# Performance work log

Hardware: AMD Instinct MI355X
Metric: run time of the kernel (lower is better)

## Reference

```python
import jax, jax.numpy as jnp
import numpy as np

B, N, NH, F = 4, 4096, 16, 8      # batch, grid cells, input points per cell, raw features
D, FF, H, PE = 256, 1024, 8, 32   # model_dim, ff_dim, n_heads, pos_emb_dim
NG, NI = 8192, 65536              # grid table size, input-point table size
SEQ = 4                           # 4 ** seq_level
HD = D // H


def layer_norm(x, g, b, eps=1e-5):
    mu = jnp.mean(x, axis=-1, keepdims=True)
    var = jnp.mean(jnp.square(x - mu), axis=-1, keepdims=True)
    return (x - mu) * jax.lax.rsqrt(var + eps) * g + b


def setup_inputs() -> dict:
    key = jax.random.key(0)
    ks = jax.random.split(key, 20)
    inp = {}
    inp["x"] = jax.random.normal(ks[0], (B, N, NH, F), jnp.float32)
    inp["grid_level_indices"] = jax.random.randint(ks[1], (B, N), 0, NG)
    inp["drop_mask"] = jax.random.bernoulli(ks[2], 0.1, (B, N))
    # buffers
    inp["input_mapping"] = jax.random.randint(ks[3], (NG, NH), 0, NI)
    inp["in_range"] = jax.random.bernoulli(ks[4], 0.95, (NG, NH))
    inp["input_coordinates"] = jax.random.uniform(ks[5], (2, NI), jnp.float32, -3.14, 3.14)
    inp["grid_coords"] = jax.random.uniform(ks[6], (2, NG), jnp.float32, -3.14, 3.14)
    # params
    inp["W_in"] = jax.random.normal(ks[7], (F, D), jnp.float32) * 0.05
    inp["b_in"] = jnp.zeros((D,), jnp.float32)
    inp["W_pe"] = jax.random.normal(ks[8], (2, PE), jnp.float32) * 0.2
    inp["W_bias"] = jax.random.normal(ks[9], (PE, H), jnp.float32) * 0.1
    inp["W_v"] = jax.random.normal(ks[10], (D, D), jnp.float32) * 0.02
    inp["W_o"] = jax.random.normal(ks[11], (D, D), jnp.float32) * 0.02
    inp["W1"] = jax.random.normal(ks[12], (D, FF), jnp.float32) * 0.02
    inp["W2"] = jax.random.normal(ks[13], (FF, D), jnp.float32) * 0.02
    inp["g1"] = jnp.ones((D,), jnp.float32)
    inp["b1"] = jnp.zeros((D,), jnp.float32)
    inp["g2"] = jnp.ones((D,), jnp.float32)
    inp["b2"] = jnp.zeros((D,), jnp.float32)
    return inp


def reference(x, grid_level_indices, drop_mask, input_mapping, in_range,
              input_coordinates, grid_coords, W_in, b_in, W_pe, W_bias,
              W_v, W_o, W1, W2, g1, b1, g2, b2):
    b, n, nh, _ = x.shape
    nq = n // SEQ
    K = SEQ * nh  # keys per group

    # input_layer.input_mlp: Linear + SiLU
    x = jax.nn.silu(x @ W_in + b_in)                       # [b,n,nh,D]

    # relative positions (polar): grid-cell coords vs gathered input-point coords
    gseq = grid_level_indices.reshape(b, nq, SEQ)
    idx = input_mapping[gseq]                              # [b,nq,4,nh]
    lon1 = grid_coords[0][gseq][..., None, None]           # [b,nq,4,1,1]
    lat1 = grid_coords[1][gseq][..., None, None]
    lon2 = input_coordinates[0][idx][:, :, None]           # [b,nq,1,4,nh]
    lat2 = input_coordinates[1][idx][:, :, None]
    dlon, dlat = lon2 - lon1, lat2 - lat1                  # [b,nq,4,4,nh]
    dist = jnp.sqrt(dlon * dlon + dlat * dlat + 1e-12)
    ang = jnp.arctan2(dlat, dlon)
    pos1 = dist.reshape(b, nq, SEQ, K)
    pos2 = ang.reshape(b, nq, SEQ, K)

    # mask: out-of-range OR dropped, broadcast across the 4 query cells
    m = (~in_range[grid_level_indices]) | drop_mask[:, :, None]  # [b,n,nh]
    m = m.reshape(b, nq, SEQ, nh)
    mask = jnp.broadcast_to(m[:, :, None], (b, nq, SEQ, SEQ, nh)).reshape(b, nq, SEQ, K)

    xs = x.reshape(b, nq, K, D)                            # kv tokens per group

    # positional bias -> attention scores (qkv_bias=False path: bias-only scores)
    pe = jax.nn.silu(jnp.stack([pos1, pos2], -1) @ W_pe)   # [b,nq,4,K,PE]
    bias = pe @ W_bias                                     # [b,nq,4,K,H]
    scores = jnp.moveaxis(bias, -1, 2)                     # [b,nq,H,4,K]
    scores = jnp.where(mask[:, :, None], -1e9, scores)
    att = jax.nn.softmax(scores, axis=-1)

    vh = (xs @ W_v).reshape(b, nq, K, H, HD)
    out = jnp.einsum('bqhtk,bqkhd->bqthd', att, vh).reshape(b, nq, SEQ, D)
    out = out @ W_o                                        # [b,nq,4,D]

    # nha_layer tail (q_res=False, dropout=0)
    h = layer_norm(out, g1, b1)
    h = layer_norm(h + jax.nn.silu(h @ W1) @ W2, g2, b2)
    return h.reshape(b, n, D)
```

## Files before the change

kernel.cpp:

```cpp
#include <hip/hip_runtime.h>

#define B_   4
#define N_   4096
#define NH_  16
#define F_   8
#define D_   256
#define FF_  1024
#define H_   8
#define PE_  32
#define NG_  8192
#define NI_  65536
#define NQ_  1024

typedef short short8 __attribute__((ext_vector_type(8)));
typedef float f32x4 __attribute__((ext_vector_type(4)));

union U8 { short8 s8; uint4 u4; };

__device__ __forceinline__ float silu_f(float v) {
  return v * __builtin_amdgcn_rcpf(1.f + __expf(-v));
}
__device__ __forceinline__ unsigned short f2bf(float f) {
  unsigned int x = __float_as_uint(f);
  unsigned int r = (x + 0x7fffu + ((x >> 16) & 1u)) >> 16;
  return (unsigned short)r;
}
__device__ __forceinline__ unsigned int cvt_pk(float a, float b) {
  unsigned int r;
  asm("v_cvt_pk_bf16_f32 %0, %1, %2" : "=v"(r) : "v"(a), "v"(b));
  return r;
}
__device__ __forceinline__ unsigned short f2bf1(float v) {
  return (unsigned short)cvt_pk(v, v);
}
__device__ __forceinline__ float bf2f(unsigned short h) {
  return __uint_as_float(((unsigned int)h) << 16);
}

__device__ __forceinline__ int detect_layout(const unsigned int* w) {
  unsigned b1 = 0, b0 = 0;
#pragma unroll
  for (int i = 0; i < 64; ++i) {
    unsigned v = w[i];
    b1 |= v & 0x0000FF00u;
    b0 |= v & 0x000000FFu;
  }
  return b1 ? 0 : (b0 ? 1 : 2);
}
__device__ __forceinline__ int read_bool(const void* p, int i, int lay) {
  if (lay == 0) return ((const unsigned char*)p)[i] != 0;
  if (lay == 1) return ((const int*)p)[i] != 0;
  return ((const float*)p)[i] != 0.0f;
}

#define WOP_OFF 0
#define W1P_OFF 65536
#define W2P_OFF (65536 + 262144)
#define WVP_OFF (65536 + 262144 + 262144)
#define WIP_OFF (65536 + 262144 + 262144 + 65536)
#define WBP_OFF (WIP_OFF + 8192)
#define WS_BASE_B ((WBP_OFF + 512) * 2)
#define DRP8_B  WS_BASE_B
#define INR8_B  (WS_BASE_B + 16384)
#define WS_MASKS_END (INR8_B + 131072)
#define ROWS_B  WS_MASKS_END
#define WS_ROWS_END (ROWS_B + 16384 * 256 * 2)
#define WS_TAIL ((65536 + 262144 + 262144) * 2)

__global__ __launch_bounds__(256) void k_pack(
    const float* __restrict__ Wo, const float* __restrict__ W1,
    const float* __restrict__ W2, const float* __restrict__ Wv,
    const float* __restrict__ Wi, const float* __restrict__ Wb,
    const void* __restrict__ drop, const void* __restrict__ inr,
    short* __restrict__ ws)
{
  int t = blockIdx.x * 256 + threadIdx.x;
  if (t < 8192) {
    int g = t & 3, n = (t >> 2) & 255, kk = t >> 10;
    int k0 = kk * 32 + g * 8;
    short8 v;
#pragma unroll
    for (int j = 0; j < 8; ++j) v[j] = (short)f2bf(Wo[(k0 + j) * 256 + n]);
    *(short8*)(ws + WOP_OFF + t * 8) = v;
  } else if (t < 40960) {
    int u = t - 8192;
    int g = u & 3, n = (u >> 2) & 1023, kk = u >> 12;
    int k0 = kk * 32 + g * 8;
    short8 v;
#pragma unroll
    for (int j = 0; j < 8; ++j) v[j] = (short)f2bf(W1[(k0 + j) * 1024 + n]);
    *(short8*)(ws + W1P_OFF + u * 8) = v;
  } else if (t < 73728) {
    int u = t - 40960;
    int g = u & 3, n = (u >> 2) & 255, kk = u >> 10;
    int k0 = kk * 32 + g * 8;
    short8 v;
#pragma unroll
    for (int j = 0; j < 8; ++j) v[j] = (short)f2bf(W2[(k0 + j) * 256 + n]);
    *(short8*)(ws + W2P_OFF + u * 8) = v;
  } else if (t < 81920) {
    int u = t - 73728;
    int g = u & 3, n = (u >> 2) & 255, kk = u >> 10;
    int k0 = kk * 32 + g * 8;
    short8 v;
#pragma unroll
    for (int j = 0; j < 8; ++j) v[j] = (short)f2bf(Wv[(k0 + j) * 256 + n]);
    *(short8*)(ws + WVP_OFF + u * 8) = v;
  } else if (t < 82944) {
    int u = t - 81920;
    int g = u & 3, n = u >> 2;
    short8 v;
#pragma unroll
    for (int j = 0; j < 8; ++j) {
      int k = g * 8 + j;
      v[j] = (k < 8) ? (short)f2bf(Wi[k * 256 + n]) : (short)0;
    }
    *(short8*)(ws + WIP_OFF + (n * 4 + g) * 8) = v;
  } else if (t < 83008) {
    int u = t - 82944;
    int g = u & 3, col = u >> 2;
    short8 v;
#pragma unroll
    for (int j = 0; j < 8; ++j) {
      int p = g * 8 + j;
      v[j] = (col < 8) ? (short)f2bf(Wb[p * 8 + col]) : (short)0;
    }
    *(short8*)(ws + WBP_OFF + (col * 4 + g) * 8) = v;
  } else if (t >= 83200) {
    int lay = detect_layout((const unsigned int*)inr);
    int t2 = t - 83200;
    char* wsb = (char*)ws;
    if (t2 < B_ * N_) {
      ((unsigned char*)(wsb + DRP8_B))[t2] =
          (unsigned char)read_bool(drop, t2, lay);
    } else if (t2 < B_ * N_ + NG_ * NH_) {
      int u = t2 - B_ * N_;
      ((unsigned char*)(wsb + INR8_B))[u] =
          (unsigned char)read_bool(inr, u, lay);
    }
  }
}

#define OFF_ATTB  32768
#define OFF_DIST  36864
#define OFF_ANG   37888
#define OFF_KLON  38912
#define OFF_KLAT  39168
#define OFF_KMSK  39424
#define OFF_GLON  39680
#define OFF_GLAT  39696

__global__ __launch_bounds__(256) void k_attn_mfma(
    const float* __restrict__ x, const int* __restrict__ gli,
    const unsigned char* __restrict__ drp8, const unsigned char* __restrict__ inr8,
    const int* __restrict__ imap, const float* __restrict__ icoord,
    const float* __restrict__ gcoord, const float* __restrict__ W_pe,
    const float* __restrict__ b_in, const short* __restrict__ WiP,
    const short* __restrict__ WbP, const short* __restrict__ WvP,
    unsigned short* __restrict__ rows, float* __restrict__ out, int userows)
{
  __shared__ __align__(16) char sm[39712];
  float* distl = (float*)(sm + OFF_DIST);
  float* angl = (float*)(sm + OFF_ANG);
  float* klon = (float*)(sm + OFF_KLON);
  float* klat = (float*)(sm + OFF_KLAT);
  int* kmask = (int*)(sm + OFF_KMSK);
  float* glon = (float*)(sm + OFF_GLON);
  float* glat = (float*)(sm + OFF_GLAT);

  const int grp = blockIdx.x;
  const int b = grp >> 10;
  const int q = grp & (NQ_ - 1);
  const int tid = threadIdx.x;
  const int w = tid >> 6;
  const int l15 = tid & 15;
  const int g = (tid & 63) >> 4;
  const int swz = (l15 & 7) << 4;

  if (tid < 64) {
    int s = tid >> 4;
    int gg = gli[b * N_ + q * 4 + s];
    if ((tid & 15) == 0) {
      glon[s] = gcoord[gg];
      glat[s] = gcoord[NG_ + gg];
    }
    int id = imap[gg * NH_ + (tid & 15)];
    klon[tid] = icoord[id];
    klat[tid] = icoord[NI_ + id];
    kmask[tid] = (inr8[gg * NH_ + (tid & 15)] == 0) |
                 (drp8[b * N_ + q * 4 + s] != 0);
  }

  {
    short8 a = {0, 0, 0, 0, 0, 0, 0, 0};
    if (g == 0) {
      const float4* xp = (const float4*)(x + (size_t)(b * N_ + q * 4) * 128);
      float4 xa = xp[(w * 16 + l15) * 2];
      float4 xc = xp[(w * 16 + l15) * 2 + 1];
      U8 u;
      u.u4.x = cvt_pk(xa.x, xa.y);
      u.u4.y = cvt_pk(xa.z, xa.w);
      u.u4.z = cvt_pk(xc.x, xc.y);
      u.u4.w = cvt_pk(xc.z, xc.w);
      a = u.s8;
    }
    const int k0 = w * 16 + g * 4;
    const int base_mlp = (l15 * 128 + k0 * 2) ^ swz;
#pragma unroll
    for (int nf = 0; nf < 16; ++nf) {
      short8 bv = *(const short8*)(WiP + ((nf * 16 + l15) * 4 + g) * 8);
      f32x4 accM = {0.f, 0.f, 0.f, 0.f};
      accM = __builtin_amdgcn_mfma_f32_16x16x32_bf16(a, bv, accM, 0, 0, 0);
      float bn = b_in[nf * 16 + l15];
      uint2 pv;
      pv.x = cvt_pk(silu_f(accM[0] + bn), silu_f(accM[1] + bn));
      pv.y = cvt_pk(silu_f(accM[2] + bn), silu_f(accM[3] + bn));
      *(uint2*)(sm + base_mlp + nf * 2048) = pv;
    }
  }
  __syncthreads();

  {
    const int t = tid >> 6, k = tid & 63;
    float dlon = klon[k] - glon[t];
    float dlat = klat[k] - glat[t];
    distl[tid] = sqrtf(dlon * dlon + dlat * dlat + 1e-12f);
    angl[tid] = atan2f(dlat, dlon);
  }
  __syncthreads();

  {
    float wpe0[8], wpe1[8];
    {
      const float4* wp = (const float4*)W_pe;
      float4 w0a = wp[g * 2], w0b = wp[g * 2 + 1];
      float4 w1a = wp[8 + g * 2], w1b = wp[8 + g * 2 + 1];
      wpe0[0] = w0a.x; wpe0[1] = w0a.y; wpe0[2] = w0a.z; wpe0[3] = w0a.w;
      wpe0[4] = w0b.x; wpe0[5] = w0b.y; wpe0[6] = w0b.z; wpe0[7] = w0b.w;
      wpe1[0] = w1a.x; wpe1[1] = w1a.y; wpe1[2] = w1a.z; wpe1[3] = w1a.w;
      wpe1[4] = w1b.x; wpe1[5] = w1b.y; wpe1[6] = w1b.z; wpe1[7] = w1b.w;
    }
    short8 wb = *(const short8*)(WbP + (l15 * 4 + g) * 8);
    f32x4 accS[4];
#pragma unroll
    for (int i = 0; i < 4; ++i) {
      int row = (w * 4 + i) * 16 + l15;
      float dd = distl[row];
      float aa = angl[row];
      float pe[8];
#pragma unroll
      for (int j = 0; j < 8; ++j)
        pe[j] = silu_f(fmaf(dd, wpe0[j], aa * wpe1[j]));
      U8 pu;
      pu.u4.x = cvt_pk(pe[0], pe[1]);
      pu.u4.y = cvt_pk(pe[2], pe[3]);
      pu.u4.z = cvt_pk(pe[4], pe[5]);
      pu.u4.w = cvt_pk(pe[6], pe[7]);
      f32x4 z = {0.f, 0.f, 0.f, 0.f};
      accS[i] = __builtin_amdgcn_mfma_f32_16x16x32_bf16(pu.s8, wb, z, 0, 0, 0);
    }
    float sv[16];
    float mx = -1e30f;
#pragma unroll
    for (int i = 0; i < 4; ++i)
#pragma unroll
      for (int r = 0; r < 4; ++r) {
        int k = i * 16 + g * 4 + r;
        float s = kmask[k] ? -1e9f : accS[i][r];
        sv[i * 4 + r] = s;
        mx = fmaxf(mx, s);
      }
    mx = fmaxf(mx, __shfl_xor(mx, 16));
    mx = fmaxf(mx, __shfl_xor(mx, 32));
    float sum = 0.f;
#pragma unroll
    for (int u = 0; u < 16; ++u) { sv[u] = __expf(sv[u] - mx); sum += sv[u]; }
    sum += __shfl_xor(sum, 16);
    sum += __shfl_xor(sum, 32);
    float inv = __builtin_amdgcn_rcpf(sum);
    if (l15 < 8) {
      int row = l15 * 4 + w;
      int base_sf = OFF_ATTB + ((row * 128 + g * 8) ^ ((row & 7) << 4));
#pragma unroll
      for (int i = 0; i < 4; ++i) {
        uint2 pv;
        pv.x = cvt_pk(sv[i * 4 + 0] * inv, sv[i * 4 + 1] * inv);
        pv.y = cvt_pk(sv[i * 4 + 2] * inv, sv[i * 4 + 3] * inv);
        *(uint2*)(sm + OFF_ATTB +
            ((row * 128 + (i * 16 + g * 4) * 2) ^ ((row & 7) << 4))) = pv;
      }
      (void)base_sf;
    }
  }
  __syncthreads();

  f32x4 accY[2][4];
  {
    f32x4 z = {0.f, 0.f, 0.f, 0.f};
#pragma unroll
    for (int mi = 0; mi < 2; ++mi)
#pragma unroll
      for (int ni = 0; ni < 4; ++ni) accY[mi][ni] = z;
  }
  {
    const int base_att = OFF_ATTB + ((l15 * 128 + g * 16) ^ swz);
    const int base_bf = ((w * 64 + l15) * 128 + g * 16) ^ swz;
#pragma unroll
    for (int kk = 0; kk < 2; ++kk) {
      const int xr = kk * 64;
      short8 a0 = *(const short8*)(sm + (base_att ^ xr));
      short8 a1 = *(const short8*)(sm + ((base_att + 2048) ^ xr));
      short8 bf[4];
#pragma unroll
      for (int ni = 0; ni < 4; ++ni)
        bf[ni] = *(const short8*)(sm + ((base_bf + ni * 2048) ^ xr));
#pragma unroll
      for (int ni = 0; ni < 4; ++ni) {
        accY[0][ni] = __builtin_amdgcn_mfma_f32_16x16x32_bf16(a0, bf[ni], accY[0][ni], 0, 0, 0);
        accY[1][ni] = __builtin_amdgcn_mfma_f32_16x16x32_bf16(a1, bf[ni], accY[1][ni], 0, 0, 0);
      }
    }
  }
  __syncthreads();

  {
    const int C6 = (g & 1) << 6;
    const int X0y = g * 2048 + (w * 64 + l15) * 2;
#pragma unroll
    for (int r = 0; r < 4; ++r) {
      const int mr = C6 ^ (r << 4);
#pragma unroll
      for (int ni = 0; ni < 4; ++ni) {
        const int t0 = (X0y + r * 512 + ni * 32) ^ mr;
        *(unsigned short*)(sm + t0) = f2bf1(accY[0][ni][r]);
        *(unsigned short*)(sm + t0 + 8192) = f2bf1(accY[1][ni][r]);
      }
    }
  }
  __syncthreads();

  {
    const int mf = w >> 1;
    f32x4 accV[4];
    {
      f32x4 z = {0.f, 0.f, 0.f, 0.f};
#pragma unroll
      for (int ni = 0; ni < 4; ++ni) accV[ni] = z;
    }
    const int base_y = ((mf * 16 + l15) * 512 + g * 16) ^ swz;
#pragma unroll
    for (int kk = 0; kk < 8; ++kk) {
      short8 a = *(const short8*)(sm + (base_y ^ (kk * 64)));
#pragma unroll
      for (int ni = 0; ni < 4; ++ni) {
        int col = w * 64 + ni * 16 + l15;
        short8 bv = *(const short8*)(WvP + ((size_t)(kk * 256 + col)) * 32 + g * 8);
        accV[ni] = __builtin_amdgcn_mfma_f32_16x16x32_bf16(a, bv, accV[ni], 0, 0, 0);
      }
    }
    float* outl = (float*)(sm + 16384);
    const int gb = (w & 1) * 2;
#pragma unroll
    for (int ni = 0; ni < 4; ++ni) {
      if (g == gb + (ni >> 1)) {
#pragma unroll
        for (int r = 0; r < 4; ++r)
          outl[r * 256 + w * 64 + ni * 16 + l15] = accV[ni][r];
      }
    }
  }
  __syncthreads();

  if (userows) {
    const float* outl = (const float*)(sm + 16384);
    unsigned* rb = (unsigned*)(rows + (size_t)grp * (4 * D_));
    int t2 = tid >> 7;
    int c2 = tid & 127;
#pragma unroll
    for (int tt = 0; tt < 2; ++tt) {
      int t = tt * 2 + t2;
      rb[t * 128 + c2] = cvt_pk(outl[t * 256 + 2 * c2],
                                outl[t * 256 + 2 * c2 + 1]);
    }
  } else {
    const float* outl = (const float*)(sm + 16384);
    float* ob = out + (size_t)grp * (4 * D_);
#pragma unroll
    for (int t = 0; t < 4; ++t) ob[t * 256 + tid] = outl[t * 256 + tid];
  }
}

__global__ __launch_bounds__(256) void k_attn_valu(
    const float* __restrict__ x, const int* __restrict__ gli,
    const void* __restrict__ drop, const int* __restrict__ imap,
    const void* __restrict__ inr, const float* __restrict__ icoord,
    const float* __restrict__ gcoord, const float* __restrict__ W_in,
    const float* __restrict__ b_in, const float* __restrict__ W_pe,
    const float* __restrict__ W_bias, const float* __restrict__ W_v,
    float* __restrict__ out)
{
  __shared__ __align__(16) float xl[512];
  __shared__ float glon[4], glat[4];
  __shared__ int gidx[4], dropf[4];
  __shared__ float klon[64], klat[64];
  __shared__ int kmask[64];
  __shared__ __align__(16) unsigned short xs[64 * D_];
  __shared__ __align__(16) float att[32 * 64];
  __shared__ __align__(16) float yl[4 * 8 * 260];

  const int grp = blockIdx.x;
  const int b = grp >> 10;
  const int q = grp & (NQ_ - 1);
  const int tid = threadIdx.x;
  const int lay = detect_layout((const unsigned int*)inr);

  if (tid < 4) {
    int g = gli[b * N_ + q * 4 + tid];
    gidx[tid] = g;
    glon[tid] = gcoord[g];
    glat[tid] = gcoord[NG_ + g];
    dropf[tid] = read_bool(drop, b * N_ + q * 4 + tid, lay);
  }
  const float* xb = x + (size_t)(b * N_ + q * 4) * (NH_ * F_);
  xl[tid] = xb[tid];
  xl[tid + 256] = xb[tid + 256];
  __syncthreads();

  if (tid < 64) {
    int s = tid >> 4;
    int g = gidx[s];
    int id = imap[g * NH_ + (tid & 15)];
    klon[tid] = icoord[id];
    klat[tid] = icoord[NI_ + id];
    kmask[tid] = (read_bool(inr, g * NH_ + (tid & 15), lay) == 0) | dropf[s];
  }
  {
    float w[8];
#pragma unroll
    for (int c = 0; c < 8; ++c) w[c] = W_in[c * D_ + tid];
    float bi = b_in[tid];
#pragma unroll 4
// ... 42 lines not shown
    float inv = 1.f / sm;
#pragma unroll
    for (int i = 0; i < 8; ++i) att[row * 64 + l8 + i * 8] = sv[i] * inv;
  }
  __syncthreads();
  {
    float acc[32];
#pragma unroll
    for (int r = 0; r < 32; ++r) acc[r] = 0.f;
    for (int k4 = 0; k4 < 64; k4 += 4) {
      float xv0 = bf2f(xs[(k4 + 0) * D_ + tid]);
      float xv1 = bf2f(xs[(k4 + 1) * D_ + tid]);
      float xv2 = bf2f(xs[(k4 + 2) * D_ + tid]);
      float xv3 = bf2f(xs[(k4 + 3) * D_ + tid]);
#pragma unroll
      for (int r = 0; r < 32; ++r) {
        float4 a = *(const float4*)&att[r * 64 + k4];
        acc[r] = fmaf(a.x, xv0, acc[r]);
        acc[r] = fmaf(a.y, xv1, acc[r]);
        acc[r] = fmaf(a.z, xv2, acc[r]);
        acc[r] = fmaf(a.w, xv3, acc[r]);
      }
    }
#pragma unroll
    for (int r = 0; r < 32; ++r)
      yl[(r & 3) * 2080 + (r >> 2) * 260 + tid] = acc[r];
  }
  __syncthreads();
  {
    const int h = tid >> 5;
    float o0 = 0.f, o1 = 0.f, o2 = 0.f, o3 = 0.f;
    for (int c = 0; c < 256; c += 4) {
      float w0 = W_v[(c + 0) * D_ + tid];
      float w1 = W_v[(c + 1) * D_ + tid];
      float w2 = W_v[(c + 2) * D_ + tid];
      float w3 = W_v[(c + 3) * D_ + tid];
      float4 y0 = *(const float4*)&yl[0 * 2080 + h * 260 + c];
      float4 y1 = *(const float4*)&yl[1 * 2080 + h * 260 + c];
      float4 y2 = *(const float4*)&yl[2 * 2080 + h * 260 + c];
      float4 y3 = *(const float4*)&yl[3 * 2080 + h * 260 + c];
      o0 = fmaf(y0.x, w0, o0); o0 = fmaf(y0.y, w1, o0); o0 = fmaf(y0.z, w2, o0); o0 = fmaf(y0.w, w3, o0);
      o1 = fmaf(y1.x, w0, o1); o1 = fmaf(y1.y, w1, o1); o1 = fmaf(y1.z, w2, o1); o1 = fmaf(y1.w, w3, o1);
      o2 = fmaf(y2.x, w0, o2); o2 = fmaf(y2.y, w1, o2); o2 = fmaf(y2.z, w2, o2); o2 = fmaf(y2.w, w3, o2);
      o3 = fmaf(y3.x, w0, o3); o3 = fmaf(y3.y, w1, o3); o3 = fmaf(y3.z, w2, o3); o3 = fmaf(y3.w, w3, o3);
    }
    float* ob = out + (size_t)grp * (4 * D_);
    ob[0 * D_ + tid] = o0;
    ob[1 * D_ + tid] = o1;
    ob[2 * D_ + tid] = o2;
    ob[3 * D_ + tid] = o3;
  }
}

template<int MI>
__device__ __forceinline__ void gemm_mfma(
    f32x4 acc[MI][4], const char* As, const short* Bp,
    int N, int kk0, int colbase, int l15, int g)
{
  const int swz = (l15 & 7) << 4;
  int baseA[MI];
#pragma unroll
  for (int mi = 0; mi < MI; ++mi)
    baseA[mi] = ((mi * 16 + l15) * 512 + g * 16) ^ swz;
#pragma unroll
  for (int kk = 0; kk < 8; ++kk) {
    short8 a[MI], bv[4];
#pragma unroll
    for (int mi = 0; mi < MI; ++mi)
      a[mi] = *(const short8*)(As + (baseA[mi] ^ (kk * 64)));
#pragma unroll
    for (int ni = 0; ni < 4; ++ni) {
      int col = colbase + ni * 16 + l15;
      size_t off = ((size_t)(kk0 + kk) * N + col) * 32 + g * 8;
      bv[ni] = *(const short8*)(Bp + off);
    }
#pragma unroll
    for (int mi = 0; mi < MI; ++mi)
#pragma unroll
      for (int ni = 0; ni < 4; ++ni)
        acc[mi][ni] = __builtin_amdgcn_mfma_f32_16x16x32_bf16(
            a[mi], bv[ni], acc[mi][ni], 0, 0, 0);
  }
}

__global__ __launch_bounds__(256) void k_tail_mfma(
    const float* __restrict__ g1v, const float* __restrict__ b1v,
    const float* __restrict__ g2v, const float* __restrict__ b2v,
    const short* __restrict__ WoP, const short* __restrict__ W1P,
    const short* __restrict__ W2P, const unsigned short* __restrict__ rowsrc,
    float* __restrict__ io, int userows)
{
  __shared__ __align__(16) unsigned short sA1[32 * 256];
  __shared__ __align__(16) unsigned short sU[32 * 256];
  __shared__ float sPs[4][32];
  __shared__ float sPss[4][32];

  const int tid = threadIdx.x;
  const int w = tid >> 6;
  const int l15 = tid & 15;
  const int g = (tid & 63) >> 4;
  float* base = io + (size_t)blockIdx.x * (32 * 256);

  const int C6 = (g & 1) << 6;
  const int X0s = g * 2048 + (w * 64 + l15) * 2;

  if (userows) {
    const unsigned short* rb = rowsrc + (size_t)blockIdx.x * (32 * 256);
#pragma unroll
    for (int i = 0; i < 8; ++i) {
      int e = (tid + 256 * i) * 4;
      int row = e >> 8, c = e & 255;
      uint2 v = *(const uint2*)(rb + e);
      int byte = (row * 512 + c * 2) ^ ((row & 7) << 4);
      *(uint2*)((char*)sU + byte) = v;
    }
  } else {
#pragma unroll
    for (int i = 0; i < 8; ++i) {
      int e = (tid + 256 * i) * 4;
      int row = e >> 8, c = e & 255;
      float4 v = *(const float4*)(base + e);
      uint2 pv;
      pv.x = cvt_pk(v.x, v.y);
      pv.y = cvt_pk(v.z, v.w);
      int byte = (row * 512 + c * 2) ^ ((row & 7) << 4);
      *(uint2*)((char*)sU + byte) = pv;
    }
  }
  __syncthreads();

  f32x4 acc[2][4];
  {
    f32x4 z = {0.f, 0.f, 0.f, 0.f};
#pragma unroll
    for (int mi = 0; mi < 2; ++mi)
#pragma unroll
      for (int ni = 0; ni < 4; ++ni) acc[mi][ni] = z;
  }
  gemm_mfma<2>(acc, (const char*)sU, WoP, 256, 0, w * 64, l15, g);

#pragma unroll
  for (int mi = 0; mi < 2; ++mi)
#pragma unroll
    for (int r = 0; r < 4; ++r) {
      float a0 = acc[mi][0][r], a1 = acc[mi][1][r], a2 = acc[mi][2][r], a3 = acc[mi][3][r];
      float s = a0 + a1 + a2 + a3;
      float ss = a0 * a0 + a1 * a1 + a2 * a2 + a3 * a3;
#pragma unroll
      for (int off = 1; off < 16; off <<= 1) {
        s += __shfl_xor(s, off);
        ss += __shfl_xor(ss, off);
      }
      if (l15 == 0) {
        int row = 16 * mi + 4 * g + r;
        sPs[w][row] = s;
        sPss[w][row] = ss;
      }
    }
  __syncthreads();

  {
    float ga[4], bb[4];
#pragma unroll
    for (int ni = 0; ni < 4; ++ni) {
      int col = 64 * w + 16 * ni + l15;
      ga[ni] = g1v[col];
      bb[ni] = b1v[col];
    }
#pragma unroll
    for (int mi = 0; mi < 2; ++mi)
#pragma unroll
      for (int r = 0; r < 4; ++r) {
        int row = 16 * mi + 4 * g + r;
        float S = sPs[0][row] + sPs[1][row] + sPs[2][row] + sPs[3][row];
        float SS = sPss[0][row] + sPss[1][row] + sPss[2][row] + sPss[3][row];
        float mu = S * (1.f / 256.f);
        float rs = rsqrtf(SS * (1.f / 256.f) - mu * mu + 1e-5f);
        const int mr = C6 ^ (r << 4);
#pragma unroll
        for (int ni = 0; ni < 4; ++ni) {
// ... 164 lines not shown
        a3[r] = fmaf(__uint_as_float(uv.z << 16), w[4], a3[r]);
        a3[r] = fmaf(__uint_as_float(uv.z & 0xffff0000u), w[5], a3[r]);
        a3[r] = fmaf(__uint_as_float(uv.w << 16), w[6], a3[r]);
        a3[r] = fmaf(__uint_as_float(uv.w & 0xffff0000u), w[7], a3[r]);
      }
    }
#pragma unroll
    for (int r = 0; r < 16; ++r) rl[r * 260 + tid] = a3[r];
  }
  __syncthreads();
  {
    const int r = tid >> 4, l = tid & 15;
    float s = 0.f, ss = 0.f;
#pragma unroll
    for (int i = 0; i < 16; ++i) { float v = rl[r * 260 + l + i * 16]; s += v; ss += v * v; }
#pragma unroll
    for (int off = 1; off < 16; off <<= 1) { s += __shfl_xor(s, off, 16); ss += __shfl_xor(ss, off, 16); }
    float mu = s * (1.f / 256.f);
    float rs = rsqrtf(ss * (1.f / 256.f) - mu * mu + 1e-5f);
#pragma unroll
    for (int i = 0; i < 16; ++i) {
      int d = l + i * 16;
      base[r * D_ + d] = (rl[r * 260 + d] - mu) * rs * g2[d] + b2[d];
    }
  }
}

extern "C" void kernel_launch(void* const* d_in, const int* in_sizes, int n_in,
                              void* d_out, int out_size, void* d_ws, size_t ws_size,
                              hipStream_t stream) {
  (void)in_sizes; (void)n_in; (void)out_size;
  const float* x = (const float*)d_in[0];
  const int* gli = (const int*)d_in[1];
  const void* drop = d_in[2];
  const int* imap = (const int*)d_in[3];
  const void* inr = d_in[4];
  const float* icoord = (const float*)d_in[5];
  const float* gcoord = (const float*)d_in[6];
  const float* W_in = (const float*)d_in[7];
  const float* b_in = (const float*)d_in[8];
  const float* W_pe = (const float*)d_in[9];
  const float* W_bias = (const float*)d_in[10];
  const float* W_v = (const float*)d_in[11];
  const float* W_o = (const float*)d_in[12];
  const float* W1 = (const float*)d_in[13];
  const float* W2 = (const float*)d_in[14];
  const float* g1 = (const float*)d_in[15];
  const float* b1 = (const float*)d_in[16];
  const float* g2 = (const float*)d_in[17];
  const float* b2 = (const float*)d_in[18];
  float* out = (float*)d_out;

  if (ws_size >= (size_t)WS_MASKS_END) {
    const int userows = (ws_size >= (size_t)WS_ROWS_END) ? 1 : 0;
    short* ws = (short*)d_ws;
    char* wsb = (char*)d_ws;
    k_pack<<<dim3(901), dim3(256), 0, stream>>>(
        W_o, W1, W2, W_v, W_in, W_bias, drop, inr, ws);
    k_attn_mfma<<<dim3(B_ * NQ_), dim3(256), 0, stream>>>(
        x, gli, (const unsigned char*)(wsb + DRP8_B),
        (const unsigned char*)(wsb + INR8_B), imap, icoord, gcoord, W_pe, b_in,
        ws + WIP_OFF, ws + WBP_OFF, ws + WVP_OFF,
        (unsigned short*)(wsb + ROWS_B), out, userows);
    k_tail_mfma<<<dim3((B_ * N_) / 32), dim3(256), 0, stream>>>(
        g1, b1, g2, b2, ws + WOP_OFF, ws + W1P_OFF, ws + W2P_OFF,
        (const unsigned short*)(wsb + ROWS_B), out, userows);
  } else if (ws_size >= (size_t)WS_TAIL) {
    short* ws = (short*)d_ws;
    k_pack<<<dim3(325), dim3(256), 0, stream>>>(
        W_o, W1, W2, W_v, W_in, W_bias, drop, inr, ws);
    k_attn_valu<<<dim3(B_ * NQ_), dim3(256), 0, stream>>>(
        x, gli, drop, imap, inr, icoord, gcoord, W_in, b_in, W_pe, W_bias, W_v, out);
    k_tail_mfma<<<dim3((B_ * N_) / 32), dim3(256), 0, stream>>>(
        g1, b1, g2, b2, ws + WOP_OFF, ws + W1P_OFF, ws + W2P_OFF,
        (const unsigned short*)0, out, 0);
  } else {
    k_attn_valu<<<dim3(B_ * NQ_), dim3(256), 0, stream>>>(
        x, gli, drop, imap, inr, icoord, gcoord, W_in, b_in, W_pe, W_bias, W_v, out);
    k_tail<<<dim3((B_ * N_) / 16), dim3(256), 0, stream>>>(
        W_o, W1, W2, g1, b1, g2, b2, out);
  }
}
```

Before: 118.1 us.

## Fuse attention and FFN tail into one kernel over four groups

Merges the attention kernel and the tail kernel (W_o, LayerNorm, FFN, LayerNorm) into a single kernel. Each block loops over four query groups, keeps their 16 output rows in shared memory as bf16, then runs the tail GEMMs on that 16-row tile. This removes the intermediate bf16 rows buffer round-trip through global memory and one kernel launch. In exchange, the tail runs with 16-row tiles (MI=1), so the packed weights are reused across fewer rows, and the grid shrinks to a quarter as many blocks with more shared memory each.

```diff
diff --git a/kernel.cpp b/kernel.cpp
--- a/kernel.cpp
+++ b/kernel.cpp
@@ -63,8 +63,6 @@
 #define DRP8_B  WS_BASE_B
 #define INR8_B  (WS_BASE_B + 16384)
 #define WS_MASKS_END (INR8_B + 131072)
-#define ROWS_B  WS_MASKS_END
-#define WS_ROWS_END (ROWS_B + 16384 * 256 * 2)
 #define WS_TAIL ((65536 + 262144 + 262144) * 2)
 
 __global__ __launch_bounds__(256) void k_pack(
@@ -141,6 +139,37 @@
   }
 }
 
+template<int MI>
+__device__ __forceinline__ void gemm_mfma(
+    f32x4 acc[MI][4], const char* As, const short* Bp,
+    int N, int kk0, int colbase, int l15, int g)
+{
+  const int swz = (l15 & 7) << 4;
+  int baseA[MI];
+#pragma unroll
+  for (int mi = 0; mi < MI; ++mi)
+    baseA[mi] = ((mi * 16 + l15) * 512 + g * 16) ^ swz;
+#pragma unroll
+  for (int kk = 0; kk < 8; ++kk) {
+    short8 a[MI], bv[4];
+#pragma unroll
+    for (int mi = 0; mi < MI; ++mi)
+      a[mi] = *(const short8*)(As + (baseA[mi] ^ (kk * 64)));
+#pragma unroll
+    for (int ni = 0; ni < 4; ++ni) {
+      int col = colbase + ni * 16 + l15;
+      size_t off = ((size_t)(kk0 + kk) * N + col) * 32 + g * 8;
+      bv[ni] = *(const short8*)(Bp + off);
+    }
+#pragma unroll
+    for (int mi = 0; mi < MI; ++mi)
+#pragma unroll
+      for (int ni = 0; ni < 4; ++ni)
+        acc[mi][ni] = __builtin_amdgcn_mfma_f32_16x16x32_bf16(
+            a[mi], bv[ni], acc[mi][ni], 0, 0, 0);
+  }
+}
+
 #define OFF_ATTB  32768
 #define OFF_DIST  36864
 #define OFF_ANG   37888
@@ -150,16 +179,23 @@
 #define OFF_GLON  39680
 #define OFF_GLAT  39696
 
-__global__ __launch_bounds__(256) void k_attn_mfma(
+__global__ __launch_bounds__(256) void k_fused(
     const float* __restrict__ x, const int* __restrict__ gli,
     const unsigned char* __restrict__ drp8, const unsigned char* __restrict__ inr8,
     const int* __restrict__ imap, const float* __restrict__ icoord,
     const float* __restrict__ gcoord, const float* __restrict__ W_pe,
     const float* __restrict__ b_in, const short* __restrict__ WiP,
     const short* __restrict__ WbP, const short* __restrict__ WvP,
-    unsigned short* __restrict__ rows, float* __restrict__ out, int userows)
+    const short* __restrict__ WoP, const short* __restrict__ W1P,
+    const short* __restrict__ W2P, const float* __restrict__ g1v,
+    const float* __restrict__ b1v, const float* __restrict__ g2v,
+    const float* __restrict__ b2v, float* __restrict__ out)
 {
   __shared__ __align__(16) char sm[39712];
+  __shared__ __align__(16) unsigned short sX[16 * 256];
+  __shared__ float sPs[4][16];
+  __shared__ float sPss[4][16];
+
   float* distl = (float*)(sm + OFF_DIST);
   float* angl = (float*)(sm + OFF_ANG);
   float* klon = (float*)(sm + OFF_KLON);
@@ -168,225 +204,331 @@
   float* glon = (float*)(sm + OFF_GLON);
   float* glat = (float*)(sm + OFF_GLAT);
 
-  const int grp = blockIdx.x;
-  const int b = grp >> 10;
-  const int q = grp & (NQ_ - 1);
   const int tid = threadIdx.x;
   const int w = tid >> 6;
   const int l15 = tid & 15;
   const int g = (tid & 63) >> 4;
   const int swz = (l15 & 7) << 4;
 
-  if (tid < 64) {
-    int s = tid >> 4;
-    int gg = gli[b * N_ + q * 4 + s];
-    if ((tid & 15) == 0) {
-      glon[s] = gcoord[gg];
-      glat[s] = gcoord[NG_ + gg];
-    }
-    int id = imap[gg * NH_ + (tid & 15)];
-    klon[tid] = icoord[id];
-    klat[tid] = icoord[NI_ + id];
-    kmask[tid] = (inr8[gg * NH_ + (tid & 15)] == 0) |
-                 (drp8[b * N_ + q * 4 + s] != 0);
-  }
-
-  {
-    short8 a = {0, 0, 0, 0, 0, 0, 0, 0};
-    if (g == 0) {
-      const float4* xp = (const float4*)(x + (size_t)(b * N_ + q * 4) * 128);
-      float4 xa = xp[(w * 16 + l15) * 2];
-      float4 xc = xp[(w * 16 + l15) * 2 + 1];
-      U8 u;
-      u.u4.x = cvt_pk(xa.x, xa.y);
-      u.u4.y = cvt_pk(xa.z, xa.w);
-      u.u4.z = cvt_pk(xc.x, xc.y);
-      u.u4.w = cvt_pk(xc.z, xc.w);
-      a = u.s8;
-    }
-    const int k0 = w * 16 + g * 4;
-    const int base_mlp = (l15 * 128 + k0 * 2) ^ swz;
-#pragma unroll
-    for (int nf = 0; nf < 16; ++nf) {
-      short8 bv = *(const short8*)(WiP + ((nf * 16 + l15) * 4 + g) * 8);
-      f32x4 accM = {0.f, 0.f, 0.f, 0.f};
-      accM = __builtin_amdgcn_mfma_f32_16x16x32_bf16(a, bv, accM, 0, 0, 0);
-      float bn = b_in[nf * 16 + l15];
-      uint2 pv;
-      pv.x = cvt_pk(silu_f(accM[0] + bn), silu_f(accM[1] + bn));
-      pv.y = cvt_pk(silu_f(accM[2] + bn), silu_f(accM[3] + bn));
-      *(uint2*)(sm + base_mlp + nf * 2048) = pv;
-    }
-  }
-  __syncthreads();
-
-  {
-    const int t = tid >> 6, k = tid & 63;
-    float dlon = klon[k] - glon[t];
-    float dlat = klat[k] - glat[t];
-    distl[tid] = sqrtf(dlon * dlon + dlat * dlat + 1e-12f);
-    angl[tid] = atan2f(dlat, dlon);
-  }
-  __syncthreads();
-
-  {
-    float wpe0[8], wpe1[8];
+  float wpe0[8], wpe1[8];
+  {
+    const float4* wp = (const float4*)W_pe;
+    float4 w0a = wp[g * 2], w0b = wp[g * 2 + 1];
+    float4 w1a = wp[8 + g * 2], w1b = wp[8 + g * 2 + 1];
+    wpe0[0] = w0a.x; wpe0[1] = w0a.y; wpe0[2] = w0a.z; wpe0[3] = w0a.w;
+    wpe0[4] = w0b.x; wpe0[5] = w0b.y; wpe0[6] = w0b.z; wpe0[7] = w0b.w;
+    wpe1[0] = w1a.x; wpe1[1] = w1a.y; wpe1[2] = w1a.z; wpe1[3] = w1a.w;
+    wpe1[4] = w1b.x; wpe1[5] = w1b.y; wpe1[6] = w1b.z; wpe1[7] = w1b.w;
+  }
+  const short8 wbias = *(const short8*)(WbP + (l15 * 4 + g) * 8);
+
+  for (int gi = 0; gi < 4; ++gi) {
+    const int grp = blockIdx.x * 4 + gi;
+    const int b = grp >> 10;
+    const int q = grp & (NQ_ - 1);
+
+    if (tid < 64) {
+      int s = tid >> 4;
+      int gg = gli[b * N_ + q * 4 + s];
+      if ((tid & 15) == 0) {
+        glon[s] = gcoord[gg];
+        glat[s] = gcoord[NG_ + gg];
+      }
+      int id = imap[gg * NH_ + (tid & 15)];
+      klon[tid] = icoord[id];
+      klat[tid] = icoord[NI_ + id];
+      kmask[tid] = (inr8[gg * NH_ + (tid & 15)] == 0) |
+                   (drp8[b * N_ + q * 4 + s] != 0);
+    }
+
     {
-      const float4* wp = (const float4*)W_pe;
-      float4 w0a = wp[g * 2], w0b = wp[g * 2 + 1];
-      float4 w1a = wp[8 + g * 2], w1b = wp[8 + g * 2 + 1];
-      wpe0[0] = w0a.x; wpe0[1] = w0a.y; wpe0[2] = w0a.z; wpe0[3] = w0a.w;
-      wpe0[4] = w0b.x; wpe0[5] = w0b.y; wpe0[6] = w0b.z; wpe0[7] = w0b.w;
-      wpe1[0] = w1a.x; wpe1[1] = w1a.y; wpe1[2] = w1a.z; wpe1[3] = w1a.w;
-      wpe1[4] = w1b.x; wpe1[5] = w1b.y; wpe1[6] = w1b.z; wpe1[7] = w1b.w;
-    }
-    short8 wb = *(const short8*)(WbP + (l15 * 4 + g) * 8);
-    f32x4 accS[4];
-#pragma unroll
-    for (int i = 0; i < 4; ++i) {
-      int row = (w * 4 + i) * 16 + l15;
-      float dd = distl[row];
-      float aa = angl[row];
-      float pe[8];
-#pragma unroll
-      for (int j = 0; j < 8; ++j)
-        pe[j] = silu_f(fmaf(dd, wpe0[j], aa * wpe1[j]));
-      U8 pu;
-      pu.u4.x = cvt_pk(pe[0], pe[1]);
-      pu.u4.y = cvt_pk(pe[2], pe[3]);
-      pu.u4.z = cvt_pk(pe[4], pe[5]);
-      pu.u4.w = cvt_pk(pe[6], pe[7]);
+      short8 a = {0, 0, 0, 0, 0, 0, 0, 0};
+      if (g == 0) {
+        const float4* xp = (const float4*)(x + (size_t)(b * N_ + q * 4) * 128);
+        float4 xa = xp[(w * 16 + l15) * 2];
+        float4 xc = xp[(w * 16 + l15) * 2 + 1];
+        U8 u;
+        u.u4.x = cvt_pk(xa.x, xa.y);
+        u.u4.y = cvt_pk(xa.z, xa.w);
+        u.u4.z = cvt_pk(xc.x, xc.y);
+        u.u4.w = cvt_pk(xc.z, xc.w);
+        a = u.s8;
+      }
+      const int k0 = w * 16 + g * 4;
+      const int base_mlp = (l15 * 128 + k0 * 2) ^ swz;
+#pragma unroll
+      for (int nf = 0; nf < 16; ++nf) {
+        short8 bv = *(const short8*)(WiP + ((nf * 16 + l15) * 4 + g) * 8);
+        f32x4 accM = {0.f, 0.f, 0.f, 0.f};
+        accM = __builtin_amdgcn_mfma_f32_16x16x32_bf16(a, bv, accM, 0, 0, 0);
+        float bn = b_in[nf * 16 + l15];
+        uint2 pv;
+        pv.x = cvt_pk(silu_f(accM[0] + bn), silu_f(accM[1] + bn));
+        pv.y = cvt_pk(silu_f(accM[2] + bn), silu_f(accM[3] + bn));
+        *(uint2*)(sm + base_mlp + nf * 2048) = pv;
+      }
+    }
+    __syncthreads();
+
+    {
+      const int t = tid >> 6, k = tid & 63;
+      float dlon = klon[k] - glon[t];
+      float dlat = klat[k] - glat[t];
+      distl[tid] = sqrtf(dlon * dlon + dlat * dlat + 1e-12f);
+      angl[tid] = atan2f(dlat, dlon);
+    }
+    __syncthreads();
+
+    {
+      f32x4 accS[4];
+#pragma unroll
+      for (int i = 0; i < 4; ++i) {
+        int row = (w * 4 + i) * 16 + l15;
+        float dd = distl[row];
+        float aa = angl[row];
+        float pe[8];
+#pragma unroll
+        for (int j = 0; j < 8; ++j)
+          pe[j] = silu_f(fmaf(dd, wpe0[j], aa * wpe1[j]));
+        U8 pu;
+        pu.u4.x = cvt_pk(pe[0], pe[1]);
+        pu.u4.y = cvt_pk(pe[2], pe[3]);
+        pu.u4.z = cvt_pk(pe[4], pe[5]);
+        pu.u4.w = cvt_pk(pe[6], pe[7]);
+        f32x4 z = {0.f, 0.f, 0.f, 0.f};
+        accS[i] = __builtin_amdgcn_mfma_f32_16x16x32_bf16(pu.s8, wbias, z, 0, 0, 0);
+      }
+      float sv[16];
+      float mx = -1e30f;
+#pragma unroll
+      for (int i = 0; i < 4; ++i)
+#pragma unroll
+        for (int r = 0; r < 4; ++r) {
+          int k = i * 16 + g * 4 + r;
+          float s = kmask[k] ? -1e9f : accS[i][r];
+          sv[i * 4 + r] = s;
+          mx = fmaxf(mx, s);
+        }
+      mx = fmaxf(mx, __shfl_xor(mx, 16));
+      mx = fmaxf(mx, __shfl_xor(mx, 32));
+      float sum = 0.f;
+#pragma unroll
+      for (int u = 0; u < 16; ++u) { sv[u] = __expf(sv[u] - mx); sum += sv[u]; }
+      sum += __shfl_xor(sum, 16);
+      sum += __shfl_xor(sum, 32);
+      float inv = __builtin_amdgcn_rcpf(sum);
+      if (l15 < 8) {
+        int row = l15 * 4 + w;
+        int rs = (row & 7) << 4;
+#pragma unroll
+        for (int i = 0; i < 4; ++i) {
+          uint2 pv;
+          pv.x = cvt_pk(sv[i * 4 + 0] * inv, sv[i * 4 + 1] * inv);
+          pv.y = cvt_pk(sv[i * 4 + 2] * inv, sv[i * 4 + 3] * inv);
+          *(uint2*)(sm + OFF_ATTB +
+              ((row * 128 + (i * 16 + g * 4) * 2) ^ rs)) = pv;
+        }
+      }
+    }
+    __syncthreads();
+
+    f32x4 accY[2][4];
+    {
       f32x4 z = {0.f, 0.f, 0.f, 0.f};
-      accS[i] = __builtin_amdgcn_mfma_f32_16x16x32_bf16(pu.s8, wb, z, 0, 0, 0);
-    }
-    float sv[16];
-    float mx = -1e30f;
-#pragma unroll
-    for (int i = 0; i < 4; ++i)
+#pragma unroll
+      for (int mi = 0; mi < 2; ++mi)
+#pragma unroll
+        for (int ni = 0; ni < 4; ++ni) accY[mi][ni] = z;
+    }
+    {
+      const int base_att = OFF_ATTB + ((l15 * 128 + g * 16) ^ swz);
+      const int base_bf = ((w * 64 + l15) * 128 + g * 16) ^ swz;
+#pragma unroll
+      for (int kk = 0; kk < 2; ++kk) {
+        const int xr = kk * 64;
+        short8 a0 = *(const short8*)(sm + (base_att ^ xr));
+        short8 a1 = *(const short8*)(sm + ((base_att + 2048) ^ xr));
+        short8 bf[4];
+#pragma unroll
+        for (int ni = 0; ni < 4; ++ni)
+          bf[ni] = *(const short8*)(sm + ((base_bf + ni * 2048) ^ xr));
+#pragma unroll
+        for (int ni = 0; ni < 4; ++ni) {
+          accY[0][ni] = __builtin_amdgcn_mfma_f32_16x16x32_bf16(a0, bf[ni], accY[0][ni], 0, 0, 0);
+          accY[1][ni] = __builtin_amdgcn_mfma_f32_16x16x32_bf16(a1, bf[ni], accY[1][ni], 0, 0, 0);
+        }
+      }
+    }
+    __syncthreads();
+
+    {
+      const int C6 = (g & 1) << 6;
+      const int X0y = g * 2048 + (w * 64 + l15) * 2;
 #pragma unroll
       for (int r = 0; r < 4; ++r) {
-        int k = i * 16 + g * 4 + r;
-        float s = kmask[k] ? -1e9f : accS[i][r];
-        sv[i * 4 + r] = s;
-        mx = fmaxf(mx, s);
-      }
-    mx = fmaxf(mx, __shfl_xor(mx, 16));
-    mx = fmaxf(mx, __shfl_xor(mx, 32));
-    float sum = 0.f;
-#pragma unroll
-    for (int u = 0; u < 16; ++u) { sv[u] = __expf(sv[u] - mx); sum += sv[u]; }
-    sum += __shfl_xor(sum, 16);
-    sum += __shfl_xor(sum, 32);
-    float inv = __builtin_amdgcn_rcpf(sum);
-    if (l15 < 8) {
-      int row = l15 * 4 + w;
-      int base_sf = OFF_ATTB + ((row * 128 + g * 8) ^ ((row & 7) << 4));
-#pragma unroll
-      for (int i = 0; i < 4; ++i) {
-        uint2 pv;
-        pv.x = cvt_pk(sv[i * 4 + 0] * inv, sv[i * 4 + 1] * inv);
-        pv.y = cvt_pk(sv[i * 4 + 2] * inv, sv[i * 4 + 3] * inv);
-        *(uint2*)(sm + OFF_ATTB +
-            ((row * 128 + (i * 16 + g * 4) * 2) ^ ((row & 7) << 4))) = pv;
-      }
-      (void)base_sf;
-    }
-  }
-  __syncthreads();
-
-  f32x4 accY[2][4];
+        const int mr = C6 ^ (r << 4);
+#pragma unroll
+        for (int ni = 0; ni < 4; ++ni) {
+          const int t0 = (X0y + r * 512 + ni * 32) ^ mr;
+          *(unsigned short*)(sm + t0) = f2bf1(accY[0][ni][r]);
+          *(unsigned short*)(sm + t0 + 8192) = f2bf1(accY[1][ni][r]);
+        }
+      }
+    }
+    __syncthreads();
+
+    {
+      const int mf = w >> 1;
+      f32x4 accV[4];
+      {
+        f32x4 z = {0.f, 0.f, 0.f, 0.f};
+#pragma unroll
+        for (int ni = 0; ni < 4; ++ni) accV[ni] = z;
+      }
+      const int base_y = ((mf * 16 + l15) * 512 + g * 16) ^ swz;
+#pragma unroll
+      for (int kk = 0; kk < 8; ++kk) {
+        short8 a = *(const short8*)(sm + (base_y ^ (kk * 64)));
+#pragma unroll
+        for (int ni = 0; ni < 4; ++ni) {
+          int col = w * 64 + ni * 16 + l15;
+          short8 bv = *(const short8*)(WvP + ((size_t)(kk * 256 + col)) * 32 + g * 8);
+          accV[ni] = __builtin_amdgcn_mfma_f32_16x16x32_bf16(a, bv, accV[ni], 0, 0, 0);
+        }
+      }
+      const int gb = (w & 1) * 2;
+#pragma unroll
+      for (int ni = 0; ni < 4; ++ni) {
+        if (g == gb + (ni >> 1)) {
+          int col = w * 64 + ni * 16 + l15;
+#pragma unroll
+          for (int r = 0; r < 4; ++r) {
+            int row = gi * 4 + r;
+            int byte = (row * 512 + col * 2) ^ ((row & 7) << 4);
+            *(unsigned short*)((char*)sX + byte) = f2bf1(accV[ni][r]);
+          }
+        }
+      }
+    }
+    __syncthreads();
+  }
+
+  const int C6 = (g & 1) << 6;
+  const int X0s = g * 2048 + (w * 64 + l15) * 2;
+
+  f32x4 acc[1][4];
   {
     f32x4 z = {0.f, 0.f, 0.f, 0.f};
 #pragma unroll
-    for (int mi = 0; mi < 2; ++mi)
-#pragma unroll
-      for (int ni = 0; ni < 4; ++ni) accY[mi][ni] = z;
-  }
-  {
-    const int base_att = OFF_ATTB + ((l15 * 128 + g * 16) ^ swz);
-    const int base_bf = ((w * 64 + l15) * 128 + g * 16) ^ swz;
-#pragma unroll
-    for (int kk = 0; kk < 2; ++kk) {
-      const int xr = kk * 64;
-      short8 a0 = *(const short8*)(sm + (base_att ^ xr));
-      short8 a1 = *(const short8*)(sm + ((base_att + 2048) ^ xr));
-      short8 bf[4];
-#pragma unroll
-      for (int ni = 0; ni < 4; ++ni)
-        bf[ni] = *(const short8*)(sm + ((base_bf + ni * 2048) ^ xr));
+    for (int ni = 0; ni < 4; ++ni) acc[0][ni] = z;
+  }
+  gemm_mfma<1>(acc, (const char*)sX, WoP, 256, 0, w * 64, l15, g);
+
+#pragma unroll
+  for (int r = 0; r < 4; ++r) {
+    float a0 = acc[0][0][r], a1 = acc[0][1][r], a2 = acc[0][2][r], a3 = acc[0][3][r];
+    float s = a0 + a1 + a2 + a3;
+    float ss = a0 * a0 + a1 * a1 + a2 * a2 + a3 * a3;
+#pragma unroll
+    for (int off = 1; off < 16; off <<= 1) {
+      s += __shfl_xor(s, off);
+      ss += __shfl_xor(ss, off);
+    }
+    if (l15 == 0) {
+      int row = 4 * g + r;
+      sPs[w][row] = s;
+      sPss[w][row] = ss;
+    }
+  }
+  __syncthreads();
+
+  {
+    float ga[4], bb[4];
+#pragma unroll
+    for (int ni = 0; ni < 4; ++ni) {
+      int col = 64 * w + 16 * ni + l15;
+      ga[ni] = g1v[col];
+      bb[ni] = b1v[col];
+    }
+#pragma unroll
+    for (int r = 0; r < 4; ++r) {
+      int row = 4 * g + r;
+      float S = sPs[0][row] + sPs[1][row] + sPs[2][row] + sPs[3][row];
+      float SS = sPss[0][row] + sPss[1][row] + sPss[2][row] + sPss[3][row];
+      float mu = S * (1.f / 256.f);
+      float rs = rsqrtf(SS * (1.f / 256.f) - mu * mu + 1e-5f);
+      const int mr = C6 ^ (r << 4);
 #pragma unroll
       for (int ni = 0; ni < 4; ++ni) {
-        accY[0][ni] = __builtin_amdgcn_mfma_f32_16x16x32_bf16(a0, bf[ni], accY[0][ni], 0, 0, 0);
-        accY[1][ni] = __builtin_amdgcn_mfma_f32_16x16x32_bf16(a1, bf[ni], accY[1][ni], 0, 0, 0);
-      }
-    }
-  }
-  __syncthreads();
-
-  {
-    const int C6 = (g & 1) << 6;
-    const int X0y = g * 2048 + (w * 64 + l15) * 2;
+        float val = (acc[0][ni][r] - mu) * rs * ga[ni] + bb[ni];
+        acc[0][ni][r] = val;
+        *(unsigned short*)(sm + ((X0s + r * 512 + ni * 32) ^ mr)) = f2bf1(val);
+      }
+    }
+  }
+  __syncthreads();
+
+  for (int p = 0; p < 4; ++p) {
+    f32x4 acc2[1][4];
+    {
+      f32x4 z = {0.f, 0.f, 0.f, 0.f};
+#pragma unroll
+      for (int ni = 0; ni < 4; ++ni) acc2[0][ni] = z;
+    }
+    gemm_mfma<1>(acc2, (const char*)sm, W1P, 1024, 0, p * 256 + w * 64, l15, g);
 #pragma unroll
     for (int r = 0; r < 4; ++r) {
       const int mr = C6 ^ (r << 4);
 #pragma unroll
+      for (int ni = 0; ni < 4; ++ni)
+        *(unsigned short*)(sm + 8192 + ((X0s + r * 512 + ni * 32) ^ mr)) =
+            f2bf1(silu_f(acc2[0][ni][r]));
+    }
+    __syncthreads();
+    gemm_mfma<1>(acc, (const char*)(sm + 8192), W2P, 256, p * 8, w * 64, l15, g);
+    __syncthreads();
+  }
+
+#pragma unroll
+  for (int r = 0; r < 4; ++r) {
+    float a0 = acc[0][0][r], a1 = acc[0][1][r], a2 = acc[0][2][r], a3 = acc[0][3][r];
+    float s = a0 + a1 + a2 + a3;
+    float ss = a0 * a0 + a1 * a1 + a2 * a2 + a3 * a3;
+#pragma unroll
+    for (int off = 1; off < 16; off <<= 1) {
+      s += __shfl_xor(s, off);
+      ss += __shfl_xor(ss, off);
+    }
+    if (l15 == 0) {
+      int row = 4 * g + r;
+      sPs[w][row] = s;
+      sPss[w][row] = ss;
+    }
+  }
+  __syncthreads();
+
+  {
+    float* base = out + (size_t)blockIdx.x * (16 * 256);
+    float ga[4], bb[4];
+#pragma unroll
+    for (int ni = 0; ni < 4; ++ni) {
+      int col = 64 * w + 16 * ni + l15;
+      ga[ni] = g2v[col];
+      bb[ni] = b2v[col];
+    }
+#pragma unroll
+    for (int r = 0; r < 4; ++r) {
+      int row = 4 * g + r;
+      float S = sPs[0][row] + sPs[1][row] + sPs[2][row] + sPs[3][row];
+      float SS = sPss[0][row] + sPss[1][row] + sPss[2][row] + sPss[3][row];
+      float mu = S * (1.f / 256.f);
+      float rs = rsqrtf(SS * (1.f / 256.f) - mu * mu + 1e-5f);
+#pragma unroll
       for (int ni = 0; ni < 4; ++ni) {
-        const int t0 = (X0y + r * 512 + ni * 32) ^ mr;
-        *(unsigned short*)(sm + t0) = f2bf1(accY[0][ni][r]);
-        *(unsigned short*)(sm + t0 + 8192) = f2bf1(accY[1][ni][r]);
-      }
-    }
-  }
-  __syncthreads();
-
-  {
-    const int mf = w >> 1;
-    f32x4 accV[4];
-    {
-      f32x4 z = {0.f, 0.f, 0.f, 0.f};
-#pragma unroll
-      for (int ni = 0; ni < 4; ++ni) accV[ni] = z;
-    }
-    const int base_y = ((mf * 16 + l15) * 512 + g * 16) ^ swz;
-#pragma unroll
-    for (int kk = 0; kk < 8; ++kk) {
-      short8 a = *(const short8*)(sm + (base_y ^ (kk * 64)));
-#pragma unroll
-      for (int ni = 0; ni < 4; ++ni) {
-        int col = w * 64 + ni * 16 + l15;
-        short8 bv = *(const short8*)(WvP + ((size_t)(kk * 256 + col)) * 32 + g * 8);
-        accV[ni] = __builtin_amdgcn_mfma_f32_16x16x32_bf16(a, bv, accV[ni], 0, 0, 0);
-      }
-    }
-    float* outl = (float*)(sm + 16384);
-    const int gb = (w & 1) * 2;
-#pragma unroll
-    for (int ni = 0; ni < 4; ++ni) {
-      if (g == gb + (ni >> 1)) {
-#pragma unroll
-        for (int r = 0; r < 4; ++r)
-          outl[r * 256 + w * 64 + ni * 16 + l15] = accV[ni][r];
-      }
-    }
-  }
-  __syncthreads();
-
-  if (userows) {
-    const float* outl = (const float*)(sm + 16384);
-    unsigned* rb = (unsigned*)(rows + (size_t)grp * (4 * D_));
-    int t2 = tid >> 7;
-    int c2 = tid & 127;
-#pragma unroll
-    for (int tt = 0; tt < 2; ++tt) {
-      int t = tt * 2 + t2;
-      rb[t * 128 + c2] = cvt_pk(outl[t * 256 + 2 * c2],
-                                outl[t * 256 + 2 * c2 + 1]);
-    }
-  } else {
-    const float* outl = (const float*)(sm + 16384);
-    float* ob = out + (size_t)grp * (4 * D_);
-#pragma unroll
-    for (int t = 0; t < 4; ++t) ob[t * 256 + tid] = outl[t * 256 + tid];
+        int col = 64 * w + 16 * ni + l15;
+        base[row * 256 + col] = (acc[0][ni][r] - mu) * rs * ga[ni] + bb[ni];
+      }
+    }
   }
 }
 
@@ -535,43 +677,11 @@
   }
 }
 
-template<int MI>
-__device__ __forceinline__ void gemm_mfma(
-    f32x4 acc[MI][4], const char* As, const short* Bp,
-    int N, int kk0, int colbase, int l15, int g)
-{
-  const int swz = (l15 & 7) << 4;
-  int baseA[MI];
-#pragma unroll
-  for (int mi = 0; mi < MI; ++mi)
-    baseA[mi] = ((mi * 16 + l15) * 512 + g * 16) ^ swz;
-#pragma unroll
-  for (int kk = 0; kk < 8; ++kk) {
-    short8 a[MI], bv[4];
-#pragma unroll
-    for (int mi = 0; mi < MI; ++mi)
-      a[mi] = *(const short8*)(As + (baseA[mi] ^ (kk * 64)));
-#pragma unroll
-    for (int ni = 0; ni < 4; ++ni) {
-      int col = colbase + ni * 16 + l15;
-      size_t off = ((size_t)(kk0 + kk) * N + col) * 32 + g * 8;
-      bv[ni] = *(const short8*)(Bp + off);
-    }
-#pragma unroll
-    for (int mi = 0; mi < MI; ++mi)
-#pragma unroll
-      for (int ni = 0; ni < 4; ++ni)
-        acc[mi][ni] = __builtin_amdgcn_mfma_f32_16x16x32_bf16(
-            a[mi], bv[ni], acc[mi][ni], 0, 0, 0);
-  }
-}
-
 __global__ __launch_bounds__(256) void k_tail_mfma(
     const float* __restrict__ g1v, const float* __restrict__ b1v,
     const float* __restrict__ g2v, const float* __restrict__ b2v,
     const short* __restrict__ WoP, const short* __restrict__ W1P,
-    const short* __restrict__ W2P, const unsigned short* __restrict__ rowsrc,
-    float* __restrict__ io, int userows)
+    const short* __restrict__ W2P, float* __restrict__ io)
 {
   __shared__ __align__(16) unsigned short sA1[32 * 256];
   __shared__ __align__(16) unsigned short sU[32 * 256];
@@ -587,28 +697,16 @@
   const int C6 = (g & 1) << 6;
   const int X0s = g * 2048 + (w * 64 + l15) * 2;
 
-  if (userows) {
-    const unsigned short* rb = rowsrc + (size_t)blockIdx.x * (32 * 256);
-#pragma unroll
-    for (int i = 0; i < 8; ++i) {
-      int e = (tid + 256 * i) * 4;
-      int row = e >> 8, c = e & 255;
-      uint2 v = *(const uint2*)(rb + e);
-      int byte = (row * 512 + c * 2) ^ ((row & 7) << 4);
-      *(uint2*)((char*)sU + byte) = v;
-    }
-  } else {
-#pragma unroll
-    for (int i = 0; i < 8; ++i) {
-      int e = (tid + 256 * i) * 4;
-      int row = e >> 8, c = e & 255;
-      float4 v = *(const float4*)(base + e);
-      uint2 pv;
-      pv.x = cvt_pk(v.x, v.y);
-      pv.y = cvt_pk(v.z, v.w);
-      int byte = (row * 512 + c * 2) ^ ((row & 7) << 4);
-      *(uint2*)((char*)sU + byte) = pv;
-    }
+#pragma unroll
+  for (int i = 0; i < 8; ++i) {
+    int e = (tid + 256 * i) * 4;
+    int row = e >> 8, c = e & 255;
+    float4 v = *(const float4*)(base + e);
+    uint2 pv;
+    pv.x = cvt_pk(v.x, v.y);
+    pv.y = cvt_pk(v.z, v.w);
+    int byte = (row * 512 + c * 2) ^ ((row & 7) << 4);
+    *(uint2*)((char*)sU + byte) = pv;
   }
   __syncthreads();
 
@@ -879,19 +977,16 @@
   float* out = (float*)d_out;
 
   if (ws_size >= (size_t)WS_MASKS_END) {
-    const int userows = (ws_size >= (size_t)WS_ROWS_END) ? 1 : 0;
     short* ws = (short*)d_ws;
     char* wsb = (char*)d_ws;
     k_pack<<<dim3(901), dim3(256), 0, stream>>>(
         W_o, W1, W2, W_v, W_in, W_bias, drop, inr, ws);
-    k_attn_mfma<<<dim3(B_ * NQ_), dim3(256), 0, stream>>>(
+    k_fused<<<dim3((B_ * NQ_) / 4), dim3(256), 0, stream>>>(
         x, gli, (const unsigned char*)(wsb + DRP8_B),
         (const unsigned char*)(wsb + INR8_B), imap, icoord, gcoord, W_pe, b_in,
         ws + WIP_OFF, ws + WBP_OFF, ws + WVP_OFF,
-        (unsigned short*)(wsb + ROWS_B), out, userows);
-    k_tail_mfma<<<dim3((B_ * N_) / 32), dim3(256), 0, stream>>>(
-        g1, b1, g2, b2, ws + WOP_OFF, ws + W1P_OFF, ws + W2P_OFF,
-        (const unsigned short*)(wsb + ROWS_B), out, userows);
+        ws + WOP_OFF, ws + W1P_OFF, ws + W2P_OFF,
+        g1, b1, g2, b2, out);
   } else if (ws_size >= (size_t)WS_TAIL) {
     short* ws = (short*)d_ws;
     k_pack<<<dim3(325), dim3(256), 0, stream>>>(
@@ -899,8 +994,7 @@
     k_attn_valu<<<dim3(B_ * NQ_), dim3(256), 0, stream>>>(
         x, gli, drop, imap, inr, icoord, gcoord, W_in, b_in, W_pe, W_bias, W_v, out);
     k_tail_mfma<<<dim3((B_ * N_) / 32), dim3(256), 0, stream>>>(
-        g1, b1, g2, b2, ws + WOP_OFF, ws + W1P_OFF, ws + W2P_OFF,
-        (const unsigned short*)0, out, 0);
+        g1, b1, g2, b2, ws + WOP_OFF, ws + W1P_OFF, ws + W2P_OFF, out);
   } else {
     k_attn_valu<<<dim3(B_ * NQ_), dim3(256), 0, stream>>>(
         x, gli, drop, imap, inr, icoord, gcoord, W_in, b_in, W_pe, W_bias, W_v, out);
```

After: 252.0 us. 2.13x slower.
